# Kernel tuning notes

Measured on AMD Instinct MI355X. Metric: run time of the kernel, lower is better.

Reference implementation:

```python
import jax, jax.numpy as jnp
import numpy as np
from math import log2

FPS = 100.0
MIN_BPM = 55.0
MAX_BPM = 215.0
NUM_TEMPI = 60
NUM_BEATS = 4
TRANS_LAMBDA = 100.0
OBS_LAMBDA = 16.0
NUM_FRAMES = 6000


def _intervals():
    mi = 60.0 * FPS / MAX_BPM
    ma = 60.0 * FPS / MIN_BPM
    iv = np.arange(round(mi), round(ma) + 1)
    if NUM_TEMPI < len(iv):
        n = NUM_TEMPI
        iv = np.zeros(0)
        while len(iv) < NUM_TEMPI:
            iv = np.unique(np.round(np.logspace(log2(mi), log2(ma), n, base=2)))
            n += 1
    return iv.astype(np.int64)


def _state_space():
    iv = _intervals()                      # (I,) tempo intervals in frames
    nsb = int(iv.sum())                    # states per beat
    first = np.concatenate([[0], np.cumsum(iv)[:-1]]).astype(np.int64)
    last = (np.cumsum(iv) - 1).astype(np.int64)
    pos_b = np.concatenate([np.arange(i) / float(i) for i in iv])
    positions = np.concatenate([pos_b + b for b in range(NUM_BEATS)])  # (S,)
    first_states = np.stack([first + b * nsb for b in range(NUM_BEATS)])  # (B,I)
    last_states = np.stack([last + b * nsb for b in range(NUM_BEATS)])    # (B,I)
    # exponential tempo transition (madmom exponential_transition, norm=True)
    ratio = iv[None, :].astype(np.float64) / iv[:, None].astype(np.float64)
    prob = np.exp(-TRANS_LAMBDA * np.abs(ratio - 1.0))
    prob[prob <= np.spacing(1)] = 0.0
    prob /= prob.sum(axis=1, keepdims=True)
    log_t = np.where(prob > 0, np.log(np.maximum(prob, 1e-300)), -1e30).astype(np.float32)
    log_trans = np.tile(log_t[None], (NUM_BEATS, 1, 1))  # same lambda per beat boundary
    prev_last = np.stack([last_states[(b - 1) % NUM_BEATS] for b in range(NUM_BEATS)])
    # observation pointers: 0 = no beat, 1 = beat, 2 = downbeat
    frac = positions % 1.0
    beat_idx = np.floor(positions).astype(np.int64)
    ptr = np.where(frac < 1.0 / OBS_LAMBDA, np.where(beat_idx == 0, 2, 1), 0)
    return first_states, prev_last, log_trans, ptr, nsb * NUM_BEATS


def setup_inputs() -> dict:
    key = jax.random.key(0)
    first_states, prev_last, log_trans, pointer, S = _state_space()
    # beat/downbeat activation probabilities; scaled so beat+downbeat < 1
    acts = jax.random.uniform(key, (NUM_FRAMES, 2), dtype=jnp.float32) * 0.45
    return {
        "activations": acts,
        "log_trans": jnp.asarray(log_trans),
        "prev_last": jnp.asarray(prev_last, dtype=jnp.int32),
        "first_states": jnp.asarray(first_states, dtype=jnp.int32),
        "pointer": jnp.asarray(pointer, dtype=jnp.int32),
        "num_states": S,
    }


def reference(activations, log_trans, prev_last, first_states, pointer, num_states):
    S = int(num_states)
    NEG = jnp.float32(-1e30)
    a_b = activations[:, 0]
    a_d = activations[:, 1]
    # log observation densities: [no-beat, beat, downbeat], shape (F, 3)
    dens = jnp.stack([
        jnp.log((1.0 - a_b - a_d) / (OBS_LAMBDA - 1.0)),
        jnp.log(a_b),
        jnp.log(a_d),
    ], axis=1)
    first_flat = first_states.reshape(-1)  # (B*I,)
    base_ptr = jnp.arange(S, dtype=jnp.int32) - 1  # default predecessor s-1

    def step(v, dens_t):
        # within-interval advance: state s comes from s-1 with prob 1
        v_shift = jnp.concatenate([jnp.full((1,), NEG, v.dtype), v[:-1]])
        # beat boundaries: first states of beat b from last states of beat b-1
        cand = v[prev_last]                      # (B, I)
        scores = cand[:, :, None] + log_trans    # (B, I_from, I_to)
        best = scores.max(axis=1).reshape(-1)    # (B*I,)
        arg = scores.argmax(axis=1)              # (B, I_to)
        bp_first = jnp.take_along_axis(prev_last, arg.astype(jnp.int32), axis=1).reshape(-1)
        ptr = base_ptr.at[first_flat].set(bp_first)
        v_new = v_shift.at[first_flat].set(best) + dens_t[pointer]
        return v_new, ptr

    v0 = jnp.full((S,), -jnp.log(jnp.float32(S)))  # uniform initial distribution
    v_final, bps = jax.lax.scan(step, v0, dens)    # bps: (F, S) backpointers
    last_state = jnp.argmax(v_final).astype(jnp.int32)
    logp = v_final[last_state]

    def back(s, bp_t):
        p = bp_t[s]
        return p, p

    _, earlier = jax.lax.scan(back, last_state, bps[1:], reverse=True)
    path = jnp.concatenate([earlier, last_state[None]])  # (F,) best state sequence
    return path, logp
```

## Files before the change

### kernel.cpp

```cpp
#include <hip/hip_runtime.h>
#include <stdint.h>


#define NB 4
#define KF 15
#define QW 16
#define BW 48
#define NPMAX 256
#define TBATCH 32
#define NEGV -1.0e30f

__device__ __forceinline__ float bf16u_to_f(uint16_t u) {
    union { uint32_t i; float f; } v; v.i = ((uint32_t)u) << 16; return v.f;
}

template<int CTRL>
__device__ __forceinline__ int dpp_i(int x) {
    return __builtin_amdgcn_update_dpp(0, x, CTRL, 0xF, 0xF, true);
}
template<int CTRL>
__device__ __forceinline__ float dpp_f(float x) {
    return __int_as_float(dpp_i<CTRL>(__float_as_int(x)));
}

__device__ __forceinline__ void load_acts(const void* p, int isbf, int t, float& a, float& d) {
    if (isbf) {
        const uint16_t* u = (const uint16_t*)p;
        uint32_t w = *(const uint32_t*)(u + 2 * t);
        a = bf16u_to_f((uint16_t)w); d = bf16u_to_f((uint16_t)(w >> 16));
    } else {
        const float2* f = (const float2*)p;
        float2 v = f[t]; a = v.x; d = v.y;
    }
}

__global__ __launch_bounds__(1024) void dbn_viterbi_v3(
    const void* __restrict__ acts_raw,
    const void* __restrict__ lt_raw,
    const int*  __restrict__ prev_last,
    const int*  __restrict__ first_states,
    float*      __restrict__ out,
    float*      __restrict__ ws_lastv,
    float*      __restrict__ ws_dens,
    int T, int S, int F)
{
    const int tid  = (int)threadIdx.x;
    const int NP   = NB * T;
    const int lane = tid & 63;
    const int wvx  = tid >> 6;

    __shared__ alignas(16) float lring[32 * 256];
    __shared__ alignas(16) float densr[64 * 4];
    __shared__ float bound2[32];
    __shared__ int   fsld[NPMAX];
    __shared__ int   plds[NPMAX];
    __shared__ int   pref[NPMAX + 1];
    __shared__ float wvs[16];
    __shared__ int   wss[16];
    __shared__ int   flag_s, mspan_s;

    if (tid == 0) {
        const uint16_t* au = (const uint16_t*)acts_raw;
        int bf = 1;
        for (int i = 0; i < 32; i++) {
            uint16_t e = au[2 * i];
            uint8_t h8 = (uint8_t)(e >> 8);
            if (!(e == 0 || (h8 >= 0x20 && h8 < 0x40))) bf = 0;
        }
        flag_s = bf; mspan_s = 0;
    }
    if (tid < NP) { fsld[tid] = first_states[tid]; plds[tid] = prev_last[tid]; }
    for (int i = tid; i < 32 * 256; i += 1024) lring[i] = NEGV;
    __syncthreads();
    const int isbf = flag_s;
    const int nsb  = S / NB;
    const uint16_t* lt_u = (const uint16_t*)lt_raw;
    const float*    lt_f = (const float*)lt_raw;

    for (int f = tid; f < F; f += 1024) {
        float ab, ad;
        load_acts(acts_raw, isbf, f, ab, ad);
        float4 r;
        r.x = logf(((1.0f - ab) - ad) / 15.0f);
        r.y = logf(ab);
        r.z = logf(ad);
        r.w = 0.0f;
        *(float4*)&ws_dens[f * 4] = r;
    }
    __threadfence();

    if (tid == 0) {
        int acc = 0;
        for (int g = 0; g < NP; g++) {
            int b = g / T, ib = g - b * T;
            int end = (ib + 1 < T) ? fsld[g + 1] : (b + 1) * nsb;
            int L = end - fsld[g];
            pref[g] = acc; acc += (L + KF - 1) / KF;
        }
        pref[NP] = acc;
    }
    __syncthreads();
    const int NT = pref[NP];

    const bool act_u = (tid < NT);
    int g_own = 0, startg = 0, Lg = 1, sb = 0, lq = 0;
    bool is_last = false, pv2 = false;
    if (act_u) {
        int lo = 0, hi = NP - 1;
        while (lo < hi) { int mid = (lo + hi + 1) >> 1; if (pref[mid] <= tid) lo = mid; else hi = mid - 1; }
        g_own = lo;
        int j = tid - pref[lo];
        int b = g_own / T, ib = g_own - b * T;
        startg = fsld[g_own];
        int end = (ib + 1 < T) ? fsld[g_own + 1] : (b + 1) * nsb;
        Lg = end - startg;
        int n = (Lg + KF - 1) / KF;
        sb = startg + Lg - KF * (n - j);
        is_last = (j == n - 1);
        lq = (b << 6) + ib;
        pv2 = (b == 0);
    }
    bool hb[KF], hq[KF];
    #pragma unroll
    for (int kk = 0; kk < KF; kk++) {
        int i = sb + kk - startg;
        hq[kk] = act_u && (i <= 0);
        hb[kk] = act_u && (16 * i < Lg);
    }

    int rowbase = 0, c0 = 0, colbase = 0;
    float ltb[BW];
    #pragma unroll
    for (int u = 0; u < BW; u++) ltb[u] = NEGV;
    if (act_u) {
        int b = g_own / T, j = g_own - (g_own / T) * T;
        rowbase = ((b + 3) & 3) << 6;
        colbase = b * T * T + j;
        int lo = T, hi = 0;
        for (int i = 0; i < T; i++) {
            float v = isbf ? bf16u_to_f(lt_u[colbase + i * T]) : lt_f[colbase + i * T];
            if (v > -1e29f) { if (i < lo) lo = i; if (i > hi) hi = i; }
        }
        if (lo > hi) { lo = 0; hi = 0; }
        atomicMax(&mspan_s, hi - lo + 1);
        c0 = lo & ~3;
        if (c0 + BW > 64) c0 = 64 - BW;
        for (int u = 0; u < BW; u++) {
            int i = c0 + u;
            if (i < T) ltb[u] = isbf ? bf16u_to_f(lt_u[colbase + i * T]) : lt_f[colbase + i * T];
        }
    }
    __syncthreads();
    const bool narrow = (mspan_s <= BW);

    const float vinit = -logf((float)S);
    float vreg[KF];
    #pragma unroll
    for (int kk = 0; kk < KF; kk++) vreg[kk] = vinit;
    if (act_u && is_last) lring[(31 << 8) + lq] = vinit;
    if (lane == 63) bound2[16 + wvx] = vinit;
    float inc_pipe = vinit;
    if (tid < 64 && tid < F) {
        float4 r = *(const float4*)&ws_dens[tid * 4];
        *(float4*)&densr[tid * 4] = r;
    }

    const int WQ = NP >> 2;
    const int TQ = T >> 2;
    __syncthreads();

    for (int t = 0; t < F; t++) {
        const float* lvR = &lring[((t + 31) & 31) << 8];
        float inc_use = inc_pipe;
        if (lane == 0) inc_use = bound2[(((t + 1) & 1) << 4) + ((wvx + 15) & 15)];

        if (wvx == 15) {
            if ((t & 31) == 0 && t >= 32 && lane < 32) {
                int fr = t + 32 + lane;
                if (fr < F) {
                    float4 r = *(const float4*)&ws_dens[fr * 4];
                    *(float4*)&densr[(fr & 63) * 4] = r;
                }
            }
            if ((t & 15) == 0 && t > 0 && lane < WQ) {
                int c = lane;
                int beat = c / TQ;
                int srcoff = 4 * c + 4 * beat;
                int t0 = t - 16;
                for (int r2 = 0; r2 < 16; r2++) {
                    int row = t0 + r2;
                    float4 v4 = *(const float4*)&lring[((row & 31) << 8) + srcoff];
                    *(float4*)&ws_lastv[(size_t)row * NP + 4 * c] = v4;
                }
            }
        }

        float bq = -INFINITY;
        if (act_u) {
            if (narrow) {
                const float* rowp = lvR + rowbase + c0;
                #pragma unroll
                for (int q4 = 0; q4 < BW / 4; q4++) {
                    float4 l = *(const float4*)(rowp + 4 * q4);
                    float m = fmaxf(fmaxf(l.x + ltb[4 * q4 + 0], l.y + ltb[4 * q4 + 1]),
                                    fmaxf(l.z + ltb[4 * q4 + 2], l.w + ltb[4 * q4 + 3]));
                    bq = fmaxf(bq, m);
                }
            } else {
                for (int i = 0; i < T; i++) {
                    float ltv = isbf ? bf16u_to_f(lt_u[colbase + i * T]) : lt_f[colbase + i * T];
                    bq = fmaxf(bq, lvR[rowbase + i] + ltv);
                }
            }
        }

        int doff = (t & 63) << 2;
        float d0  = densr[doff];
        float dpv = densr[doff + (pv2 ? 2 : 1)];
        #pragma unroll
        for (int kk = KF - 1; kk >= 0; kk--) {
            float prev = (kk == 0) ? inc_use : vreg[kk - 1];
            prev = hq[kk] ? bq : prev;
            float add = hb[kk] ? dpv : d0;
            vreg[kk] = prev + add;
        }
        if (act_u && is_last) lring[((t & 31) << 8) + lq] = vreg[KF - 1];
        if (lane == 63) bound2[((t & 1) << 4) + wvx] = vreg[KF - 1];
        inc_pipe = __shfl_up(vreg[KF - 1], 1, 64);

        __syncthreads();
    }

    if (wvx == 15 && lane < WQ) {
        int lastf = (F - 1) & ~15;
        int c = lane;
        int beat = c / TQ;
        int srcoff = 4 * c + 4 * beat;
        for (int row = lastf; row <= F - 2; row++) {
            float4 v4 = *(const float4*)&lring[((row & 31) << 8) + srcoff];
            *(float4*)&ws_lastv[(size_t)row * NP + 4 * c] = v4;
        }
        __threadfence();
    }

    float mv = -INFINITY; int ms = 0x7FFFFFFF;
    #pragma unroll
    for (int kk = 0; kk < KF; kk++) {
        int s = sb + kk;
        bool valid = act_u && (s >= startg);
        float v = vreg[kk];
        if (valid && v > mv) { mv = v; ms = s; }
    }
    #pragma unroll
    for (int d = 1; d < 64; d <<= 1) {
        float ov = __shfl_xor(mv, d, 64);
        int   os = __shfl_xor(ms, d, 64);
        if (ov > mv || (ov == mv && os < ms)) { mv = ov; ms = os; }
    }
    if (lane == 0) { wvs[wvx] = mv; wss[wvx] = ms; }
    __syncthreads();

    if (tid == 0) {
        float bm = -INFINITY; int bs = 0x7FFFFFFF;
        for (int w = 0; w < 16; w++) {
            if (wvs[w] > bm || (wvs[w] == bm && wss[w] < bs)) { bm = wvs[w]; bs = wss[w]; }
        }
        int s = bs;
        int t = F - 1;
        out[F - 1] = (float)s;
        while (t > 0) {
            int b = s / nsb;
            int lo = b * T, hi = b * T + T - 1;
            while (lo < hi) { int mid = (lo + hi + 1) >> 1; if (fsld[mid] <= s) lo = mid; else hi = mid - 1; }
            int p = lo;
            int run = s - fsld[p];
            if (run == 0) {
                int jt = p - b * T;
                int pb = (b + 3) & 3;
                const float* lrow = &ws_lastv[(size_t)(t - 1) * NP + pb * T];
                float bmv = -INFINITY; int ai = 0;
                for (int i = 0; i < T; i++) {
                    int idx = (b * T + i) * T + jt;
                    float ltv = isbf ? bf16u_to_f(lt_u[idx]) : lt_f[idx];
                    float sc = lrow[i] + ltv;
                    if (sc > bmv) { bmv = sc; ai = i; }
                }
                s = plds[b * T + ai];
                out[t - 1] = (float)s;
                t--;
            } else {
                int m = (run < t) ? run : t;
                for (int jj = 0; jj < m; jj++) out[t - 1 - jj] = (float)(s - 1 - jj);
                s -= m; t -= m;
            }
        }
        out[F] = bm;
    }
}

__global__ __launch_bounds__(1024) void dbn_viterbi_v1(
    const void* __restrict__ acts_raw, const void* __restrict__ lt_raw,
    const int* __restrict__ prev_last, const int* __restrict__ first_states,
    float* __restrict__ out, uint8_t* __restrict__ ws_argi,
    int T, int S, int F)
{
    const int tid  = (int)threadIdx.x;
    const int NP   = NB * T;
    const int lane = tid & 63;
    const int wvx  = tid >> 6;

    __shared__ alignas(16) float lastv2[2 * NB * 64];
    __shared__ float bestv[NPMAX];
    __shared__ float bound[16];
    __shared__ int   fsld[NPMAX];
    __shared__ int   plds[NPMAX];
    __shared__ int   pref[NPMAX + 1];
    __shared__ float dens_s[4];
    __shared__ float wvs[16];
    __shared__ int   wss[16];
    __shared__ int   flag_s;
    __shared__ uint8_t argi_s[TBATCH * 240 + 16];

    if (tid == 0) {
        const uint16_t* au = (const uint16_t*)acts_raw;
        int bf = 1;
        for (int i = 0; i < 32; i++) {
            uint16_t e = au[2 * i];
            uint8_t h8 = (uint8_t)(e >> 8);
            if (!(e == 0 || (h8 >= 0x20 && h8 < 0x40))) bf = 0;
        }
        flag_s = bf;
    }
    if (tid < NP)          { fsld[tid] = first_states[tid]; plds[tid] = prev_last[tid]; }
    if (tid < 2 * NB * 64) lastv2[tid] = NEGV;
    __syncthreads();
    const int isbf = flag_s;
    const int nsb  = S / NB;
    const uint16_t* lt_u = (const uint16_t*)lt_raw;
    const float*    lt_f = (const float*)lt_raw;

    if (tid == 0) {
        int acc = 0;
        for (int g = 0; g < NP; g++) {
            int b = g / T, ib = g - b * T;
            int end = (ib + 1 < T) ? fsld[g + 1] : (b + 1) * nsb;
            int L = end - fsld[g];
            pref[g] = acc; acc += (L + KF - 1) / KF;
        }
        pref[NP] = acc;
    }
    __syncthreads();
    const int NT = pref[NP];

    const bool act_u = (tid < NT);
    int g_own = 0, startg = 0, Lg = 1, sb = 0, lq = 0;
    bool is_last = false, pv2 = false;
    if (act_u) {
        int lo = 0, hi = NP - 1;
        while (lo < hi) { int mid = (lo + hi + 1) >> 1; if (pref[mid] <= tid) lo = mid; else hi = mid - 1; }
        g_own = lo;
        int j = tid - pref[lo];
        int b = g_own / T, ib = g_own - b * T;
        startg = fsld[g_own];
        int end = (ib + 1 < T) ? fsld[g_own + 1] : (b + 1) * nsb;
        Lg = end - startg;
        int n = (Lg + KF - 1) / KF;
        sb = startg + Lg - KF * (n - j);
        is_last = (j == n - 1);
        lq = (b << 6) + ib;
        pv2 = (b == 0);
    }
    bool hb[KF], hq[KF];
    #pragma unroll
    for (int kk = 0; kk < KF; kk++) {
        int i = sb + kk - startg;
        hq[kk] = act_u && (i <= 0);
        hb[kk] = act_u && (16 * i < Lg);
    }

    const int g_a = tid >> 2, k4 = tid & 3;
    const bool act_g = (g_a < NP);
    float ltreg[QW];
    #pragma unroll
    for (int u = 0; u < QW; u++) ltreg[u] = NEGV;
    int rowbase = 0;
    if (act_g) {
        int b = g_a / T, j = g_a - (g_a / T) * T;
        rowbase = ((b + 3) & 3) << 6;
        #pragma unroll
        for (int u = 0; u < QW; u++) {
            int i = k4 * QW + u;
            if (i < T) {
                int idx = (b * T + i) * T + j;
                ltreg[u] = isbf ? bf16u_to_f(lt_u[idx]) : lt_f[idx];
            }
        }
    }

    const float vinit = -logf((float)S);
    float vreg[KF];
    #pragma unroll
    for (int kk = 0; kk < KF; kk++) vreg[kk] = vinit;
    if (act_u && is_last) lastv2[256 + lq] = vinit;
    if (lane == 63) bound[wvx] = vinit;
    float inc_pipe = vinit;
    float ab_c = 0.0f, ad_c = 0.0f;
    if (wvx == 15 && lane >= 60 && lane < 63) load_acts(acts_raw, isbf, 0, ab_c, ad_c);

    for (int t = 0; t < F; t++) {
        __syncthreads();
        const float* lvR = lastv2 + (((t & 1) ^ 1) << 8);
        float inc_use = inc_pipe;
        if (lane == 0) inc_use = bound[(wvx + 15) & 15];

        if (wvx == 15) {
            if (lane >= 60 && lane < 63) {
                int c3 = lane - 60;
                float dv = (c3 == 0) ? logf(((1.0f - ab_c) - ad_c) / 15.0f)
                         : (c3 == 1) ? logf(ab_c) : logf(ad_c);
                dens_s[c3] = dv;
                if (t + 1 < F) load_acts(acts_raw, isbf, t + 1, ab_c, ad_c);
            }
        } else if (act_g) {
            const float* rowp = &lvR[rowbase + k4 * QW];
            float4 l0 = *(const float4*)(rowp + 0);
            float4 l1 = *(const float4*)(rowp + 4);
            float4 l2 = *(const float4*)(rowp + 8);
            float4 l3 = *(const float4*)(rowp + 12);
            float cand[QW] = { l0.x, l0.y, l0.z, l0.w, l1.x, l1.y, l1.z, l1.w,
                               l2.x, l2.y, l2.z, l2.w, l3.x, l3.y, l3.z, l3.w };
            float mv = -INFINITY; int ai = 0;
            #pragma unroll
            for (int u = 0; u < QW; u++) {
                float sc = cand[u] + ltreg[u];
                if (sc > mv) { mv = sc; ai = k4 * QW + u; }
            }
            float ov = dpp_f<0xB1>(mv); int oa = dpp_i<0xB1>(ai);
            if (ov > mv || (ov == mv && oa < ai)) { mv = ov; ai = oa; }
            ov = dpp_f<0x4E>(mv); oa = dpp_i<0x4E>(ai);
            if (ov > mv || (ov == mv && oa < ai)) { mv = ov; ai = oa; }
            if (k4 == 0) {
                bestv[g_a] = mv;
                argi_s[(t & (TBATCH - 1)) * NP + g_a] = (uint8_t)ai;
            }
        }

        __syncthreads();
        float d0  = dens_s[0];
        float dpv = pv2 ? dens_s[2] : dens_s[1];
        float bq  = bestv[g_own];
        #pragma unroll
        for (int kk = KF - 1; kk >= 0; kk--) {
            float prev = (kk == 0) ? inc_use : vreg[kk - 1];
            prev = hq[kk] ? bq : prev;
            float add = hb[kk] ? dpv : d0;
            vreg[kk] = prev + add;
        }
        float* lvW = lastv2 + ((t & 1) << 8);
        if (act_u && is_last) lvW[lq] = vreg[KF - 1];
        if (lane == 63) bound[wvx] = vreg[KF - 1];
        inc_pipe = __shfl_up(vreg[KF - 1], 1, 64);

        int tB = t & (TBATCH - 1);
        if (tB == TBATCH - 1 || t == F - 1) {
            int nbytes = (tB + 1) * NP;
            int t0 = t - tB;
            for (int off = tid * 4; off < nbytes; off += 4096) {
                uint32_t w = *(const uint32_t*)&argi_s[off];
                *(uint32_t*)&ws_argi[(size_t)t0 * NP + off] = w;
            }
        }
    }

    __syncthreads();
    float mv = -INFINITY; int ms = 0x7FFFFFFF;
    #pragma unroll
    for (int kk = 0; kk < KF; kk++) {
        int s = sb + kk;
        bool valid = act_u && (s >= startg);
        float v = vreg[kk];
        if (valid && v > mv) { mv = v; ms = s; }
    }
    #pragma unroll
    for (int d = 1; d < 64; d <<= 1) {
        float ov = __shfl_xor(mv, d, 64);
        int   os = __shfl_xor(ms, d, 64);
        if (ov > mv || (ov == mv && os < ms)) { mv = ov; ms = os; }
    }
    if (lane == 0) { wvs[wvx] = mv; wss[wvx] = ms; }
    __syncthreads();

    if (tid == 0) {
        float bm = -INFINITY; int bs = 0x7FFFFFFF;
        for (int w = 0; w < 16; w++) {
            if (wvs[w] > bm || (wvs[w] == bm && wss[w] < bs)) { bm = wvs[w]; bs = wss[w]; }
        }
        int s = bs;
        int t = F - 1;
        out[F - 1] = (float)s;
        while (t > 0) {
            int b = s / nsb;
            int lo = b * T, hi = b * T + T - 1;
            while (lo < hi) { int mid = (lo + hi + 1) >> 1; if (fsld[mid] <= s) lo = mid; else hi = mid - 1; }
            int p = lo;
            int run = s - fsld[p];
            if (run == 0) {
                int ai = ws_argi[(size_t)t * NP + p];
                s = plds[b * T + ai];
                out[t - 1] = (float)s;
                t--;
            } else {
                int m = (run < t) ? run : t;
                for (int jj = 0; jj < m; jj++) out[t - 1 - jj] = (float)(s - 1 - jj);
                s -= m; t -= m;
            }
        }
        out[F] = bm;
    }
}

extern "C" void kernel_launch(void* const* d_in, const int* in_sizes, int n_in,
                              void* d_out, int out_size, void* d_ws, size_t ws_size,
                              hipStream_t stream) {
    const int F  = in_sizes[0] / 2;
    const int NP = in_sizes[2];
    const int T  = NP / NB;
    const int S  = in_sizes[4];

    const size_t need3 = ((size_t)F * NP + 4 * (size_t)F) * 4;
    const bool okgeom = ((T & 3) == 0) && (NP <= NPMAX) && (T <= 64) && (F >= 2);
    const bool fast3  = okgeom && (ws_size >= need3);

    if (fast3) {
        float* ws_lv = (float*)d_ws;
        float* ws_de = ws_lv + (size_t)F * NP;
        hipLaunchKernelGGL(dbn_viterbi_v3, dim3(1), dim3(1024), 0, stream,
                           d_in[0], d_in[1],
                           (const int*)d_in[2], (const int*)d_in[3],
                           (float*)d_out, ws_lv, ws_de, T, S, F);
    } else {
        hipLaunchKernelGGL(dbn_viterbi_v1, dim3(1), dim3(1024), 0, stream,
                           d_in[0], d_in[1],
                           (const int*)d_in[2], (const int*)d_in[3],
                           (float*)d_out, (uint8_t*)d_ws, T, S, F);
    }
}
```

Before: 7.222 ms.

## Split Viterbi block into boundary-max and chain-update waves with one-step lag

The single 1024-thread block is split by role. Four waves compute the beat-boundary max per tempo into a double-buffered shared array, and twelve waves advance the chain states, now 24 per thread instead of 15. The boundary result is applied one step late through a patch value, so the max and chain work overlap within one barrier per step instead of sitting in series. The lastv spill to global memory is spread across all waves. The new path is gated on exact problem geometry (T=60, NP=240, S=12288), so other shapes fall back to the older kernel.

```diff
diff --git a/kernel.cpp b/kernel.cpp
--- a/kernel.cpp
+++ b/kernel.cpp
@@ -4,8 +4,10 @@
 
 #define NB 4
 #define KF 15
+#define KF4 24
+#define AOFF 256
+#define BW2 40
 #define QW 16
-#define BW 48
 #define NPMAX 256
 #define TBATCH 32
 #define NEGV -1.0e30f
@@ -13,16 +15,6 @@
 __device__ __forceinline__ float bf16u_to_f(uint16_t u) {
     union { uint32_t i; float f; } v; v.i = ((uint32_t)u) << 16; return v.f;
 }
-
-template<int CTRL>
-__device__ __forceinline__ int dpp_i(int x) {
-    return __builtin_amdgcn_update_dpp(0, x, CTRL, 0xF, 0xF, true);
-}
-template<int CTRL>
-__device__ __forceinline__ float dpp_f(float x) {
-    return __int_as_float(dpp_i<CTRL>(__float_as_int(x)));
-}
-
 __device__ __forceinline__ void load_acts(const void* p, int isbf, int t, float& a, float& d) {
     if (isbf) {
         const uint16_t* u = (const uint16_t*)p;
@@ -34,7 +26,7 @@
     }
 }
 
-__global__ __launch_bounds__(1024) void dbn_viterbi_v3(
+__global__ __launch_bounds__(1024) void dbn_viterbi_v4(
     const void* __restrict__ acts_raw,
     const void* __restrict__ lt_raw,
     const int*  __restrict__ prev_last,
@@ -51,13 +43,14 @@
 
     __shared__ alignas(16) float lring[32 * 256];
     __shared__ alignas(16) float densr[64 * 4];
+    __shared__ float bestp2[2 * 256];
     __shared__ float bound2[32];
     __shared__ int   fsld[NPMAX];
     __shared__ int   plds[NPMAX];
     __shared__ int   pref[NPMAX + 1];
     __shared__ float wvs[16];
     __shared__ int   wss[16];
-    __shared__ int   flag_s, mspan_s;
+    __shared__ int   flag_s, span_s;
 
     if (tid == 0) {
         const uint16_t* au = (const uint16_t*)acts_raw;
@@ -67,10 +60,11 @@
             uint8_t h8 = (uint8_t)(e >> 8);
             if (!(e == 0 || (h8 >= 0x20 && h8 < 0x40))) bf = 0;
         }
-        flag_s = bf; mspan_s = 0;
+        flag_s = bf; span_s = 0;
     }
     if (tid < NP) { fsld[tid] = first_states[tid]; plds[tid] = prev_last[tid]; }
     for (int i = tid; i < 32 * 256; i += 1024) lring[i] = NEGV;
+    if (tid < 32) bound2[tid] = 0.0f;
     __syncthreads();
     const int isbf = flag_s;
     const int nsb  = S / NB;
@@ -88,176 +82,182 @@
         *(float4*)&ws_dens[f * 4] = r;
     }
     __threadfence();
-
     if (tid == 0) {
         int acc = 0;
         for (int g = 0; g < NP; g++) {
             int b = g / T, ib = g - b * T;
             int end = (ib + 1 < T) ? fsld[g + 1] : (b + 1) * nsb;
             int L = end - fsld[g];
-            pref[g] = acc; acc += (L + KF - 1) / KF;
+            pref[g] = acc; acc += (L + KF4 - 1) / KF4;
         }
         pref[NP] = acc;
     }
     __syncthreads();
     const int NT = pref[NP];
-
-    const bool act_u = (tid < NT);
-    int g_own = 0, startg = 0, Lg = 1, sb = 0, lq = 0;
-    bool is_last = false, pv2 = false;
-    if (act_u) {
-        int lo = 0, hi = NP - 1;
-        while (lo < hi) { int mid = (lo + hi + 1) >> 1; if (pref[mid] <= tid) lo = mid; else hi = mid - 1; }
-        g_own = lo;
-        int j = tid - pref[lo];
-        int b = g_own / T, ib = g_own - b * T;
-        startg = fsld[g_own];
-        int end = (ib + 1 < T) ? fsld[g_own + 1] : (b + 1) * nsb;
-        Lg = end - startg;
-        int n = (Lg + KF - 1) / KF;
-        sb = startg + Lg - KF * (n - j);
-        is_last = (j == n - 1);
-        lq = (b << 6) + ib;
-        pv2 = (b == 0);
-    }
-    bool hb[KF], hq[KF];
-    #pragma unroll
-    for (int kk = 0; kk < KF; kk++) {
-        int i = sb + kk - startg;
-        hq[kk] = act_u && (i <= 0);
-        hb[kk] = act_u && (16 * i < Lg);
-    }
-
-    int rowbase = 0, c0 = 0, colbase = 0;
-    float ltb[BW];
-    #pragma unroll
-    for (int u = 0; u < BW; u++) ltb[u] = NEGV;
-    if (act_u) {
-        int b = g_own / T, j = g_own - (g_own / T) * T;
-        rowbase = ((b + 3) & 3) << 6;
-        colbase = b * T * T + j;
-        int lo = T, hi = 0;
-        for (int i = 0; i < T; i++) {
-            float v = isbf ? bf16u_to_f(lt_u[colbase + i * T]) : lt_f[colbase + i * T];
-            if (v > -1e29f) { if (i < lo) lo = i; if (i > hi) hi = i; }
-        }
-        if (lo > hi) { lo = 0; hi = 0; }
-        atomicMax(&mspan_s, hi - lo + 1);
-        c0 = lo & ~3;
-        if (c0 + BW > 64) c0 = 64 - BW;
-        for (int u = 0; u < BW; u++) {
-            int i = c0 + u;
-            if (i < T) ltb[u] = isbf ? bf16u_to_f(lt_u[colbase + i * T]) : lt_f[colbase + i * T];
-        }
-    }
-    __syncthreads();
-    const bool narrow = (mspan_s <= BW);
-
     const float vinit = -logf((float)S);
-    float vreg[KF];
-    #pragma unroll
-    for (int kk = 0; kk < KF; kk++) vreg[kk] = vinit;
-    if (act_u && is_last) lring[(31 << 8) + lq] = vinit;
-    if (lane == 63) bound2[16 + wvx] = vinit;
-    float inc_pipe = vinit;
-    if (tid < 64 && tid < F) {
-        float4 r = *(const float4*)&ws_dens[tid * 4];
-        *(float4*)&densr[tid * 4] = r;
-    }
-
-    const int WQ = NP >> 2;
-    const int TQ = T >> 2;
-    __syncthreads();
-
-    for (int t = 0; t < F; t++) {
-        const float* lvR = &lring[((t + 31) & 31) << 8];
-        float inc_use = inc_pipe;
-        if (lane == 0) inc_use = bound2[(((t + 1) & 1) << 4) + ((wvx + 15) & 15)];
-
-        if (wvx == 15) {
-            if ((t & 31) == 0 && t >= 32 && lane < 32) {
-                int fr = t + 32 + lane;
+    const int WQ = NP >> 2, TQ = T >> 2;
+
+    if (tid < AOFF) {
+        const int b = wvx, j = lane;
+        const bool act_a = (j < T);
+        const int rowbase = ((b + 3) & 3) << 6;
+        const int dsel = (b == 0) ? 2 : 1;
+        int c0 = 0, colbase = 0;
+        float ltb[BW2];
+        #pragma unroll
+        for (int u = 0; u < BW2; u++) ltb[u] = NEGV;
+        if (act_a) {
+            colbase = b * T * T + j;
+            int lo = T, hi = 0;
+            for (int i = 0; i < T; i++) {
+                float v = isbf ? bf16u_to_f(lt_u[colbase + i * T]) : lt_f[colbase + i * T];
+                if (v > -1e29f) { if (i < lo) lo = i; if (i > hi) hi = i; }
+            }
+            if (lo > hi) { lo = 0; hi = 0; }
+            atomicMax(&span_s, hi - lo + 1);
+            c0 = lo & ~3;
+            if (c0 > 64 - BW2) c0 = 64 - BW2;
+            for (int u = 0; u < BW2; u++) {
+                int i = c0 + u;
+                if (i < T) ltb[u] = isbf ? bf16u_to_f(lt_u[colbase + i * T]) : lt_f[colbase + i * T];
+            }
+        }
+        if (tid < 256) bestp2[256 + tid] = vinit;
+        if (tid < 64 && tid < F) {
+            float4 r = *(const float4*)&ws_dens[tid * 4];
+            *(float4*)&densr[tid * 4] = r;
+        }
+        __syncthreads();
+        const bool narrow = (span_s <= 37);
+
+        for (int t = 0; t < F; t++) {
+            if ((t & 15) == 0 && t >= 16 && lane < WQ) {
+                int row = t - 16 + wvx;
+                int c = lane, beat = c / TQ;
+                float4 v4 = *(const float4*)&lring[((row & 31) << 8) + 4 * c + 4 * beat];
+                *(float4*)&ws_lastv[(size_t)row * NP + 4 * c] = v4;
+            }
+            if (act_a) {
+                const float* lvR = &lring[((t + 31) & 31) << 8];
+                float mvv = -INFINITY;
+                if (narrow) {
+                    const float* rp = lvR + rowbase + c0;
+                    #pragma unroll
+                    for (int q = 0; q < BW2 / 4; q++) {
+                        float4 l = *(const float4*)(rp + 4 * q);
+                        mvv = fmaxf(mvv, fmaxf(fmaxf(l.x + ltb[4*q+0], l.y + ltb[4*q+1]),
+                                               fmaxf(l.z + ltb[4*q+2], l.w + ltb[4*q+3])));
+                    }
+                } else {
+                    for (int i = 0; i < T; i++) {
+                        float ltv = isbf ? bf16u_to_f(lt_u[colbase + i * T]) : lt_f[colbase + i * T];
+                        mvv = fmaxf(mvv, lvR[rowbase + i] + ltv);
+                    }
+                }
+                bestp2[((t & 1) << 8) + b * T + j] = mvv + densr[((t & 63) << 2) + dsel];
+            }
+            __syncthreads();
+        }
+        if (lane == 0) { wvs[wvx] = -INFINITY; wss[wvx] = 0x7FFFFFFF; }
+    } else {
+        const int ut = tid - AOFF;
+        const int uw = wvx - 4;
+        const bool act_u = (ut < NT);
+        int g_own = 0, startg = 0, Lg = 1, sb = 0, lq = 0, kk_head = -1;
+        bool is_last = false, pv2 = false, pred_is_head = false;
+        if (act_u) {
+            int lo = 0, hi = NP - 1;
+            while (lo < hi) { int mid = (lo + hi + 1) >> 1; if (pref[mid] <= ut) lo = mid; else hi = mid - 1; }
+            g_own = lo;
+            int j = ut - pref[lo];
+            int b = g_own / T, ib = g_own - b * T;
+            startg = fsld[g_own];
+            int end = (ib + 1 < T) ? fsld[g_own + 1] : (b + 1) * nsb;
+            Lg = end - startg;
+            int n = (Lg + KF4 - 1) / KF4;
+            sb = startg + Lg - KF4 * (n - j);
+            is_last = (j == n - 1);
+            lq = (b << 6) + ib;
+            pv2 = (b == 0);
+            int i0 = sb - startg;
+            kk_head = (i0 <= 0) ? (-i0) : -1;
+            pred_is_head = (i0 == 1);
+        }
+        bool hb[KF4], hpp[KF4];
+        #pragma unroll
+        for (int kk = 0; kk < KF4; kk++) {
+            int i = (sb - startg) + kk;
+            hb[kk]  = act_u && (16 * i < Lg);
+            hpp[kk] = act_u && (kk >= 1) && (i == 1);
+        }
+        float vreg[KF4];
+        #pragma unroll
+        for (int kk = 0; kk < KF4; kk++) vreg[kk] = vinit;
+        if (act_u && is_last) lring[(31 << 8) + lq] = vinit;
+        if (lane == 63) bound2[16 + uw] = vinit;
+        __syncthreads();
+
+        for (int t = 0; t < F; t++) {
+            if ((t & 15) == 0 && t >= 16 && lane < WQ) {
+                int row = t - 16 + wvx;
+                int c = lane, beat = c / TQ;
+                float4 v4 = *(const float4*)&lring[((row & 31) << 8) + 4 * c + 4 * beat];
+                *(float4*)&ws_lastv[(size_t)row * NP + 4 * c] = v4;
+            }
+            if (wvx == 14 && (t & 31) == 0 && t >= 32 && lane < 32) {
+                int fr = t + 31 + lane;
                 if (fr < F) {
                     float4 r = *(const float4*)&ws_dens[fr * 4];
                     *(float4*)&densr[(fr & 63) * 4] = r;
                 }
             }
-            if ((t & 15) == 0 && t > 0 && lane < WQ) {
-                int c = lane;
-                int beat = c / TQ;
-                int srcoff = 4 * c + 4 * beat;
-                int t0 = t - 16;
-                for (int r2 = 0; r2 < 16; r2++) {
-                    int row = t0 + r2;
-                    float4 v4 = *(const float4*)&lring[((row & 31) << 8) + srcoff];
-                    *(float4*)&ws_lastv[(size_t)row * NP + 4 * c] = v4;
-                }
-            }
-        }
-
-        float bq = -INFINITY;
-        if (act_u) {
-            if (narrow) {
-                const float* rowp = lvR + rowbase + c0;
-                #pragma unroll
-                for (int q4 = 0; q4 < BW / 4; q4++) {
-                    float4 l = *(const float4*)(rowp + 4 * q4);
-                    float m = fmaxf(fmaxf(l.x + ltb[4 * q4 + 0], l.y + ltb[4 * q4 + 1]),
-                                    fmaxf(l.z + ltb[4 * q4 + 2], l.w + ltb[4 * q4 + 3]));
-                    bq = fmaxf(bq, m);
-                }
-            } else {
-                for (int i = 0; i < T; i++) {
-                    float ltv = isbf ? bf16u_to_f(lt_u[colbase + i * T]) : lt_f[colbase + i * T];
-                    bq = fmaxf(bq, lvR[rowbase + i] + ltv);
-                }
-            }
-        }
-
-        int doff = (t & 63) << 2;
-        float d0  = densr[doff];
-        float dpv = densr[doff + (pv2 ? 2 : 1)];
+            float sh = __shfl_up(vreg[KF4 - 1], 1, 64);
+            float patchv = bestp2[(((t + 1) & 1) << 8) + g_own];
+            float4 dn = *(const float4*)&densr[(t & 63) << 2];
+            float d0 = dn.x;
+            float dpv = pv2 ? dn.z : dn.y;
+            float inc = (lane == 0) ? bound2[(((t + 1) & 1) << 4) + ((uw + 15) & 15)] : sh;
+            inc = pred_is_head ? patchv : inc;
+            #pragma unroll
+            for (int kk = KF4 - 1; kk >= 0; kk--) {
+                float prev = (kk == 0) ? inc : vreg[kk - 1];
+                prev = hpp[kk] ? patchv : prev;
+                float add = hb[kk] ? dpv : d0;
+                vreg[kk] = prev + add;
+            }
+            if (act_u && is_last) lring[((t & 31) << 8) + lq] = vreg[KF4 - 1];
+            if (lane == 63) bound2[((t & 1) << 4) + uw] = vreg[KF4 - 1];
+            __syncthreads();
+        }
+
+        float patchF = bestp2[(((F - 1) & 1) << 8) + g_own];
+        float mv = -INFINITY; int ms = 0x7FFFFFFF;
         #pragma unroll
-        for (int kk = KF - 1; kk >= 0; kk--) {
-            float prev = (kk == 0) ? inc_use : vreg[kk - 1];
-            prev = hq[kk] ? bq : prev;
-            float add = hb[kk] ? dpv : d0;
-            vreg[kk] = prev + add;
-        }
-        if (act_u && is_last) lring[((t & 31) << 8) + lq] = vreg[KF - 1];
-        if (lane == 63) bound2[((t & 1) << 4) + wvx] = vreg[KF - 1];
-        inc_pipe = __shfl_up(vreg[KF - 1], 1, 64);
-
-        __syncthreads();
-    }
-
-    if (wvx == 15 && lane < WQ) {
-        int lastf = (F - 1) & ~15;
-        int c = lane;
-        int beat = c / TQ;
-        int srcoff = 4 * c + 4 * beat;
-        for (int row = lastf; row <= F - 2; row++) {
-            float4 v4 = *(const float4*)&lring[((row & 31) << 8) + srcoff];
+        for (int kk = 0; kk < KF4; kk++) {
+            int s = sb + kk;
+            float v = (kk == kk_head) ? patchF : vreg[kk];
+            if (act_u && s >= startg && v > mv) { mv = v; ms = s; }
+        }
+        #pragma unroll
+        for (int d = 1; d < 64; d <<= 1) {
+            float ov = __shfl_xor(mv, d, 64);
+            int   os = __shfl_xor(ms, d, 64);
+            if (ov > mv || (ov == mv && os < ms)) { mv = ov; ms = os; }
+        }
+        if (lane == 0) { wvs[wvx] = mv; wss[wvx] = ms; }
+    }
+
+    __syncthreads();
+    {
+        int t0 = (F - 1) & ~15;
+        int row = t0 + wvx;
+        if (row <= F - 2 && lane < WQ) {
+            int c = lane, beat = c / TQ;
+            float4 v4 = *(const float4*)&lring[((row & 31) << 8) + 4 * c + 4 * beat];
             *(float4*)&ws_lastv[(size_t)row * NP + 4 * c] = v4;
         }
         __threadfence();
     }
-
-    float mv = -INFINITY; int ms = 0x7FFFFFFF;
-    #pragma unroll
-    for (int kk = 0; kk < KF; kk++) {
-        int s = sb + kk;
-        bool valid = act_u && (s >= startg);
-        float v = vreg[kk];
-        if (valid && v > mv) { mv = v; ms = s; }
-    }
-    #pragma unroll
-    for (int d = 1; d < 64; d <<= 1) {
-        float ov = __shfl_xor(mv, d, 64);
-        int   os = __shfl_xor(ms, d, 64);
-        if (ov > mv || (ov == mv && os < ms)) { mv = ov; ms = os; }
-    }
-    if (lane == 0) { wvs[wvx] = mv; wss[wvx] = ms; }
     __syncthreads();
 
     if (tid == 0) {
@@ -298,10 +298,19 @@
     }
 }
 
-__global__ __launch_bounds__(1024) void dbn_viterbi_v1(
+template<int CTRL>
+__device__ __forceinline__ int dpp_i(int x) {
+    return __builtin_amdgcn_update_dpp(0, x, CTRL, 0xF, 0xF, true);
+}
+template<int CTRL>
+__device__ __forceinline__ float dpp_f(float x) {
+    return __int_as_float(dpp_i<CTRL>(__float_as_int(x)));
+}
+
+__global__ __launch_bounds__(1024) void dbn_viterbi_v2(
     const void* __restrict__ acts_raw, const void* __restrict__ lt_raw,
     const int* __restrict__ prev_last, const int* __restrict__ first_states,
-    float* __restrict__ out, uint8_t* __restrict__ ws_argi,
+    float* __restrict__ out, float* __restrict__ ws_lastv, float* __restrict__ ws_dens,
     int T, int S, int F)
 {
     const int tid  = (int)threadIdx.x;
@@ -309,17 +318,16 @@
     const int lane = tid & 63;
     const int wvx  = tid >> 6;
 
-    __shared__ alignas(16) float lastv2[2 * NB * 64];
+    __shared__ alignas(16) float lring[32 * 256];
+    __shared__ alignas(16) float densr[64 * 4];
     __shared__ float bestv[NPMAX];
     __shared__ float bound[16];
     __shared__ int   fsld[NPMAX];
     __shared__ int   plds[NPMAX];
     __shared__ int   pref[NPMAX + 1];
-    __shared__ float dens_s[4];
     __shared__ float wvs[16];
     __shared__ int   wss[16];
-    __shared__ int   flag_s;
-    __shared__ uint8_t argi_s[TBATCH * 240 + 16];
+    __shared__ int   flag_s, mspan_s;
 
     if (tid == 0) {
         const uint16_t* au = (const uint16_t*)acts_raw;
@@ -329,16 +337,27 @@
             uint8_t h8 = (uint8_t)(e >> 8);
             if (!(e == 0 || (h8 >= 0x20 && h8 < 0x40))) bf = 0;
         }
-        flag_s = bf;
-    }
-    if (tid < NP)          { fsld[tid] = first_states[tid]; plds[tid] = prev_last[tid]; }
-    if (tid < 2 * NB * 64) lastv2[tid] = NEGV;
+        flag_s = bf; mspan_s = 0;
+    }
+    if (tid < NP) { fsld[tid] = first_states[tid]; plds[tid] = prev_last[tid]; }
+    for (int i = tid; i < 32 * 256; i += 1024) lring[i] = NEGV;
     __syncthreads();
     const int isbf = flag_s;
     const int nsb  = S / NB;
     const uint16_t* lt_u = (const uint16_t*)lt_raw;
     const float*    lt_f = (const float*)lt_raw;
 
+    for (int f = tid; f < F; f += 1024) {
+        float ab, ad;
+        load_acts(acts_raw, isbf, f, ab, ad);
+        float4 r;
+        r.x = logf(((1.0f - ab) - ad) / 15.0f);
+        r.y = logf(ab);
+        r.z = logf(ad);
+        r.w = 0.0f;
+        *(float4*)&ws_dens[f * 4] = r;
+    }
+    __threadfence();
     if (tid == 0) {
         int acc = 0;
         for (int g = 0; g < NP; g++) {
@@ -380,18 +399,33 @@
 
     const int g_a = tid >> 2, k4 = tid & 3;
     const bool act_g = (g_a < NP);
+    int rowbase = 0, lo_b = 0, b_a = 0, j_a = 0;
+    if (act_g) {
+        b_a = g_a / T; j_a = g_a - b_a * T;
+        rowbase = ((b_a + 3) & 3) << 6;
+        int lo = T, hi = 0;
+        for (int i = 0; i < T; i++) {
+            int idx = (b_a * T + i) * T + j_a;
+            float v = isbf ? bf16u_to_f(lt_u[idx]) : lt_f[idx];
+            if (v > -1e29f) { if (i < lo) lo = i; hi = i; }
+        }
+        lo_b = lo;
+        if (k4 == 0) atomicMax(&mspan_s, hi - lo + 1);
+    }
+    __syncthreads();
+    const bool banded = (mspan_s <= 44);
     float ltreg[QW];
     #pragma unroll
     for (int u = 0; u < QW; u++) ltreg[u] = NEGV;
-    int rowbase = 0;
+    int cb = 0;
     if (act_g) {
-        int b = g_a / T, j = g_a - (g_a / T) * T;
-        rowbase = ((b + 3) & 3) << 6;
-        #pragma unroll
-        for (int u = 0; u < QW; u++) {
-            int i = k4 * QW + u;
+        if (banded) { cb = (lo_b & ~3) + 12 * k4; if (cb > 52) cb = 52; }
+        else cb = 16 * k4;
+        const int nu = banded ? 12 : 16;
+        for (int u = 0; u < nu; u++) {
+            int i = cb + u;
             if (i < T) {
-                int idx = (b * T + i) * T + j;
+                int idx = (b_a * T + i) * T + j_a;
                 ltreg[u] = isbf ? bf16u_to_f(lt_u[idx]) : lt_f[idx];
             }
         }
@@ -401,53 +435,65 @@
     float vreg[KF];
     #pragma unroll
     for (int kk = 0; kk < KF; kk++) vreg[kk] = vinit;
-    if (act_u && is_last) lastv2[256 + lq] = vinit;
+    if (act_u && is_last) lring[(31 << 8) + lq] = vinit;
     if (lane == 63) bound[wvx] = vinit;
     float inc_pipe = vinit;
-    float ab_c = 0.0f, ad_c = 0.0f;
-    if (wvx == 15 && lane >= 60 && lane < 63) load_acts(acts_raw, isbf, 0, ab_c, ad_c);
+    if (tid < 64 && tid < F) {
+        float4 r = *(const float4*)&ws_dens[tid * 4];
+        *(float4*)&densr[tid * 4] = r;
+    }
+    const int WQ = NP >> 2, TQ = T >> 2;
 
     for (int t = 0; t < F; t++) {
         __syncthreads();
-        const float* lvR = lastv2 + (((t & 1) ^ 1) << 8);
+        const float* lvR = &lring[((t + 31) & 31) << 8];
         float inc_use = inc_pipe;
         if (lane == 0) inc_use = bound[(wvx + 15) & 15];
 
         if (wvx == 15) {
-            if (lane >= 60 && lane < 63) {
-                int c3 = lane - 60;
-                float dv = (c3 == 0) ? logf(((1.0f - ab_c) - ad_c) / 15.0f)
-                         : (c3 == 1) ? logf(ab_c) : logf(ad_c);
-                dens_s[c3] = dv;
-                if (t + 1 < F) load_acts(acts_raw, isbf, t + 1, ab_c, ad_c);
+            if ((t & 31) == 0 && t >= 32 && lane < 32) {
+                int fr = t + 32 + lane;
+                if (fr < F) {
+                    float4 r = *(const float4*)&ws_dens[fr * 4];
+                    *(float4*)&densr[(fr & 63) * 4] = r;
+                }
+            }
+            if ((t & 15) == 0 && t > 0 && lane < WQ) {
+                int c = lane, beat = c / TQ;
+                int srcoff = 4 * c + 4 * beat, t0 = t - 16;
+                for (int r2 = 0; r2 < 16; r2++) {
+                    int row = t0 + r2;
+                    float4 v4 = *(const float4*)&lring[((row & 31) << 8) + srcoff];
+                    *(float4*)&ws_lastv[(size_t)row * NP + 4 * c] = v4;
+                }
             }
         } else if (act_g) {
-            const float* rowp = &lvR[rowbase + k4 * QW];
+            const float* rowp = lvR + rowbase + cb;
             float4 l0 = *(const float4*)(rowp + 0);
             float4 l1 = *(const float4*)(rowp + 4);
             float4 l2 = *(const float4*)(rowp + 8);
-            float4 l3 = *(const float4*)(rowp + 12);
-            float cand[QW] = { l0.x, l0.y, l0.z, l0.w, l1.x, l1.y, l1.z, l1.w,
-                               l2.x, l2.y, l2.z, l2.w, l3.x, l3.y, l3.z, l3.w };
-            float mv = -INFINITY; int ai = 0;
-            #pragma unroll
-            for (int u = 0; u < QW; u++) {
-                float sc = cand[u] + ltreg[u];
-                if (sc > mv) { mv = sc; ai = k4 * QW + u; }
-            }
-            float ov = dpp_f<0xB1>(mv); int oa = dpp_i<0xB1>(ai);
-            if (ov > mv || (ov == mv && oa < ai)) { mv = ov; ai = oa; }
-            ov = dpp_f<0x4E>(mv); oa = dpp_i<0x4E>(ai);
-            if (ov > mv || (ov == mv && oa < ai)) { mv = ov; ai = oa; }
-            if (k4 == 0) {
-                bestv[g_a] = mv;
-                argi_s[(t & (TBATCH - 1)) * NP + g_a] = (uint8_t)ai;
-            }
+            float m0 = fmaxf(fmaxf(l0.x + ltreg[0], l0.y + ltreg[1]),
+                             fmaxf(l0.z + ltreg[2], l0.w + ltreg[3]));
+            float m1 = fmaxf(fmaxf(l1.x + ltreg[4], l1.y + ltreg[5]),
+                             fmaxf(l1.z + ltreg[6], l1.w + ltreg[7]));
+            float m2 = fmaxf(fmaxf(l2.x + ltreg[8], l2.y + ltreg[9]),
+                             fmaxf(l2.z + ltreg[10], l2.w + ltreg[11]));
+            float mv = fmaxf(fmaxf(m0, m1), m2);
+            if (!banded) {
+                float4 l3 = *(const float4*)(rowp + 12);
+                float m3 = fmaxf(fmaxf(l3.x + ltreg[12], l3.y + ltreg[13]),
+                                 fmaxf(l3.z + ltreg[14], l3.w + ltreg[15]));
+                mv = fmaxf(mv, m3);
+            }
+            mv = fmaxf(mv, dpp_f<0xB1>(mv));
+            mv = fmaxf(mv, dpp_f<0x4E>(mv));
+            if (k4 == 0) bestv[g_a] = mv;
         }
 
         __syncthreads();
-        float d0  = dens_s[0];
-        float dpv = pv2 ? dens_s[2] : dens_s[1];
+        int doff = (t & 63) << 2;
+        float d0  = densr[doff];
+        float dpv = densr[doff + (pv2 ? 2 : 1)];
         float bq  = bestv[g_own];
         #pragma unroll
         for (int kk = KF - 1; kk >= 0; kk--) {
@@ -456,23 +502,23 @@
             float add = hb[kk] ? dpv : d0;
             vreg[kk] = prev + add;
         }
-        float* lvW = lastv2 + ((t & 1) << 8);
-        if (act_u && is_last) lvW[lq] = vreg[KF - 1];
+        if (act_u && is_last) lring[((t & 31) << 8) + lq] = vreg[KF - 1];
         if (lane == 63) bound[wvx] = vreg[KF - 1];
         inc_pipe = __shfl_up(vreg[KF - 1], 1, 64);
-
-        int tB = t & (TBATCH - 1);
-        if (tB == TBATCH - 1 || t == F - 1) {
-            int nbytes = (tB + 1) * NP;
-            int t0 = t - tB;
-            for (int off = tid * 4; off < nbytes; off += 4096) {
-                uint32_t w = *(const uint32_t*)&argi_s[off];
-                *(uint32_t*)&ws_argi[(size_t)t0 * NP + off] = w;
-            }
-        }
-    }
-
-    __syncthreads();
+    }
+
+    __syncthreads();
+    if (wvx == 15 && lane < WQ) {
+        int lastf = (F - 1) & ~15;
+        int c = lane, beat = c / TQ;
+        int srcoff = 4 * c + 4 * beat;
+        for (int row = lastf; row <= F - 2; row++) {
+            float4 v4 = *(const float4*)&lring[((row & 31) << 8) + srcoff];
+            *(float4*)&ws_lastv[(size_t)row * NP + 4 * c] = v4;
+        }
+        __threadfence();
+    }
+
     float mv = -INFINITY; int ms = 0x7FFFFFFF;
     #pragma unroll
     for (int kk = 0; kk < KF; kk++) {
@@ -505,7 +551,16 @@
             int p = lo;
             int run = s - fsld[p];
             if (run == 0) {
-                int ai = ws_argi[(size_t)t * NP + p];
+                int jt = p - b * T;
+                int pb = (b + 3) & 3;
+                const float* lrow = &ws_lastv[(size_t)(t - 1) * NP + pb * T];
+                float bmv = -INFINITY; int ai = 0;
+                for (int i = 0; i < T; i++) {
+                    int idx = (b * T + i) * T + jt;
+                    float ltv = isbf ? bf16u_to_f(lt_u[idx]) : lt_f[idx];
+                    float sc = lrow[i] + ltv;
+                    if (sc > bmv) { bmv = sc; ai = i; }
+                }
                 s = plds[b * T + ai];
                 out[t - 1] = (float)s;
                 t--;
@@ -527,21 +582,22 @@
     const int T  = NP / NB;
     const int S  = in_sizes[4];
 
-    const size_t need3 = ((size_t)F * NP + 4 * (size_t)F) * 4;
-    const bool okgeom = ((T & 3) == 0) && (NP <= NPMAX) && (T <= 64) && (F >= 2);
-    const bool fast3  = okgeom && (ws_size >= need3);
-
-    if (fast3) {
-        float* ws_lv = (float*)d_ws;
-        float* ws_de = ws_lv + (size_t)F * NP;
-        hipLaunchKernelGGL(dbn_viterbi_v3, dim3(1), dim3(1024), 0, stream,
+    const size_t need = ((size_t)F * NP + 4 * (size_t)F) * 4;
+    float* ws_lv = (float*)d_ws;
+    float* ws_de = ws_lv + (size_t)F * NP;
+
+    const bool okv4 = (T == 60) && (NP == 240) && (S == 12288) && (F >= 64) && (ws_size >= need);
+    const bool okv2 = ((T & 3) == 0) && (NP <= NPMAX) && (T <= 64) && (F >= 2) && (ws_size >= need);
+
+    if (okv4) {
+        hipLaunchKernelGGL(dbn_viterbi_v4, dim3(1), dim3(1024), 0, stream,
                            d_in[0], d_in[1],
                            (const int*)d_in[2], (const int*)d_in[3],
                            (float*)d_out, ws_lv, ws_de, T, S, F);
-    } else {
-        hipLaunchKernelGGL(dbn_viterbi_v1, dim3(1), dim3(1024), 0, stream,
+    } else if (okv2) {
+        hipLaunchKernelGGL(dbn_viterbi_v2, dim3(1), dim3(1024), 0, stream,
                            d_in[0], d_in[1],
                            (const int*)d_in[2], (const int*)d_in[3],
-                           (float*)d_out, (uint8_t*)d_ws, T, S, F);
+                           (float*)d_out, ws_lv, ws_de, T, S, F);
     }
 }
```

Result: faster. 6.336 ms (-12.3%).
